# Kernel tuning notes

Measured on AMD Instinct MI355X. Metric: run time of the kernel, lower is better.

Reference implementation:

```python
import jax, jax.numpy as jnp
import numpy as np

EMBED_DIM = 2048
NUM_HEADS = 16
HEAD_DIM = EMBED_DIM // NUM_HEADS
WINDOW = 512  # window_size; also used as chunk size (S must be a multiple)


def setup_inputs() -> dict:
    key = jax.random.key(0)
    k1, k2, k3 = jax.random.split(key, 3)
    B, S = 2, 4096
    x = jax.random.normal(k1, (B, S, EMBED_DIM), dtype=jnp.float32)
    w_qkv = jax.random.normal(k2, (3 * EMBED_DIM, EMBED_DIM), dtype=jnp.float32) * 0.02
    w_out = jax.random.normal(k3, (EMBED_DIM, EMBED_DIM), dtype=jnp.float32) * 0.02
    return {"x": x, "w_qkv": w_qkv, "w_out": w_out}


def _sliding_window_attn(q, k, v, window):
    # q,k,v: [B,H,S,d]; causal sliding window: kv valid iff 0 <= q_idx - kv_idx <= window.
    # Chunked O(S*window): each query chunk of size C=window attends to its own
    # chunk and the previous one (exactly covers the band of width window+1).
    B, H, S, d = q.shape
    C = window
    nc = S // C
    qc = q.reshape(B, H, nc, C, d)

    def two_chunks(t):
        tc = t.reshape(B, H, nc, C, d)
        prev = jnp.pad(tc[:, :, :-1], ((0, 0), (0, 0), (1, 0), (0, 0), (0, 0)))
        return jnp.concatenate([prev, tc], axis=3)  # [B,H,nc,2C,d]

    kc = two_chunks(k)
    vc = two_chunks(v)

    scale = 1.0 / np.sqrt(d).astype(np.float32)
    scores = jnp.einsum('bhnid,bhnjd->bhnij', qc, kc) * scale  # [B,H,nc,C,2C]

    i = jnp.arange(C)[:, None]            # local query index
    j = jnp.arange(2 * C)[None, :]        # local kv index within the 2-chunk span
    band = (j >= i) & (j <= i + C)        # causal & within window (C == window)
    kv_global = (jnp.arange(nc)[:, None, None] - 1) * C + j[None]  # [nc,1,2C]
    mask = band[None] & (kv_global >= 0)  # [nc,C,2C]; drops padded chunk 0 keys

    scores = jnp.where(mask[None, None], scores, jnp.finfo(scores.dtype).min)
    probs = jax.nn.softmax(scores, axis=-1)
    out = jnp.einsum('bhnij,bhnjd->bhnid', probs, vc)  # [B,H,nc,C,d]
    return out.reshape(B, H, S, d)


def reference(x, w_qkv, w_out):
    B, S, E = x.shape
    qkv = jnp.einsum('bse,fe->bsf', x, w_qkv)                       # [B,S,3E]
    qkv = qkv.reshape(B, S, 3, NUM_HEADS, HEAD_DIM)
    qkv = jnp.transpose(qkv, (2, 0, 3, 1, 4))                        # [3,B,H,S,d]
    q, k, v = qkv[0], qkv[1], qkv[2]
    attn = _sliding_window_attn(q, k, v, WINDOW)                     # [B,H,S,d]
    attn = jnp.transpose(attn, (0, 2, 1, 3)).reshape(B, S, E)
    return jnp.einsum('bse,fe->bsf', attn, w_out)
```

## Files before the change

### kernel.cpp

```cpp
#include <hip/hip_runtime.h>
#include <hip/hip_bf16.h>
#include <math.h>


#define SEQ   4096
#define BATCH 2
#define EMBED 2048
#define HEADS 16
#define HDIM  128
#define NELEM (BATCH * SEQ * EMBED)
#define SCL2E (0.088388347648318447f * 1.4426950408889634f)

typedef __attribute__((ext_vector_type(8))) short short8;
typedef __attribute__((ext_vector_type(4))) float f32x4;

__device__ __forceinline__ unsigned short f2bf(float f) {
    unsigned int u = __float_as_uint(f);
    u = (u + 0x7fff + ((u >> 16) & 1)) >> 16;
    return (unsigned short)u;
}

__device__ __forceinline__ unsigned int cvt_pk_bf16(float a, float b) {
    unsigned int r;
    asm volatile("v_cvt_pk_bf16_f32 %0, %1, %2" : "=v"(r) : "v"(a), "v"(b));
    return r;
}

__global__ void cast_bf16_kernel(const float* __restrict__ src,
                                 unsigned short* __restrict__ dst, int n8)
{
    const int i = blockIdx.x * blockDim.x + threadIdx.x;
    if (i >= n8) return;
    const float4 v0 = ((const float4*)src)[2 * i];
    const float4 v1 = ((const float4*)src)[2 * i + 1];
    union { unsigned short us[8]; uint4 u4; } o;
    o.us[0] = f2bf(v0.x); o.us[1] = f2bf(v0.y); o.us[2] = f2bf(v0.z); o.us[3] = f2bf(v0.w);
    o.us[4] = f2bf(v1.x); o.us[5] = f2bf(v1.y); o.us[6] = f2bf(v1.z); o.us[7] = f2bf(v1.w);
    ((uint4*)dst)[i] = o.u4;
}

template <int MODE>
__global__ __launch_bounds__(512, 2)
void gemm256_kernel(const unsigned short* __restrict__ A,
                    const unsigned short* __restrict__ B,
                    float* __restrict__ C,
                    unsigned short* __restrict__ P0,
                    unsigned short* __restrict__ P1,
                    int M, int N, int K)
{
    __shared__ __align__(16) char lds[131072];

    const int tid  = threadIdx.x;
    const int lane = tid & 63;
    const int w    = tid >> 6;
    const int wm   = w >> 2;
    const int wn   = w & 3;
    const int l16  = lane & 15;
    const int kg   = lane >> 4;

    const int nwg  = gridDim.x * gridDim.y;
    const int bidl = blockIdx.y * gridDim.x + blockIdx.x;
    const int cpx  = nwg >> 3;
    const int swzb = (bidl & 7) * cpx + (bidl >> 3);
    const int MB   = gridDim.y;
    const int n0   = (swzb / MB) * 256;
    const int m0   = (swzb % MB) * 256;

    const int srow = w * 8 + (lane >> 3);
    const int sch8 = ((lane & 7) ^ (lane >> 3)) * 8;

    auto stage = [&](const unsigned short* X, int rowbase, int t2, int ldsbase) {
#pragma unroll
        for (int u = 0; u < 2; ++u) {
            const unsigned short* g = X + (size_t)(rowbase + u * 64 + srow) * K
                                      + t2 * 64 + sch8;
            unsigned int lb = __builtin_amdgcn_readfirstlane(
                (unsigned int)(uintptr_t)(lds + ldsbase + u * 8192 + w * 1024));
            asm volatile("s_mov_b32 m0, %0\n\t"
                         "global_load_lds_dwordx4 %1, off"
                         :: "s"(lb), "v"(g) : "memory");
        }
    };
    auto rdA = [&](int p, int mf, int ks) -> short8 {
        return *(const short8*)(lds + p * 32768 + (wm * 128 + mf * 16 + l16) * 128
                                + (((ks * 4 + kg) ^ (l16 & 7)) << 4));
    };
    auto rdB = [&](int p, int nf, int ks) -> short8 {
        return *(const short8*)(lds + 65536 + p * 32768
                                + (wn * 64 + nf * 16 + l16) * 128
                                + (((ks * 4 + kg) ^ (l16 & 7)) << 4));
    };

    f32x4 acc[8][4];
#pragma unroll
    for (int i = 0; i < 8; ++i)
#pragma unroll
        for (int j = 0; j < 4; ++j) acc[i][j] = (f32x4)0.f;

    const int NT = K >> 6;

    stage(A, m0 + 0,   0, 0);
    stage(A, m0 + 128, 0, 16384);
    stage(B, n0 + 0,   0, 65536);
    stage(B, n0 + 128, 0, 65536 + 16384);
    if (NT > 1) {
        stage(B, n0 + 0,   1, 65536 + 32768);
        stage(B, n0 + 128, 1, 65536 + 32768 + 16384);
        asm volatile("s_waitcnt vmcnt(4)" ::: "memory");
    } else {
        asm volatile("s_waitcnt vmcnt(0)" ::: "memory");
    }
    asm volatile("s_barrier" ::: "memory");

    short8 afrA[2][2], afrB[2][2], bfr[4][2];
#pragma unroll
    for (int i = 0; i < 2; ++i)
#pragma unroll
        for (int ks = 0; ks < 2; ++ks) afrA[i][ks] = rdA(0, i, ks);
#pragma unroll
    for (int nf = 0; nf < 4; ++nf)
#pragma unroll
        for (int ks = 0; ks < 2; ++ks) bfr[nf][ks] = rdB(0, nf, ks);

#define MFMA_QUAD(Q, FR)                                                        \
    __builtin_amdgcn_s_setprio(1);                                              \
    _Pragma("unroll")                                                           \
    for (int i = 0; i < 2; ++i)                                                 \
        _Pragma("unroll")                                                       \
        for (int nf = 0; nf < 4; ++nf)                                          \
            _Pragma("unroll")                                                   \
            for (int ks = 0; ks < 2; ++ks)                                      \
                acc[2 * (Q) + i][nf] = __builtin_amdgcn_mfma_f32_16x16x32_bf16( \
                    FR[i][ks], bfr[nf][ks], acc[2 * (Q) + i][nf], 0, 0, 0);     \
    __builtin_amdgcn_s_setprio(0);

    for (int t = 0; t < NT; ++t) {
        const int p = t & 1;
        if (t + 1 < NT) stage(A, m0 + 0, t + 1, (p ^ 1) * 32768);
        asm volatile("s_barrier" ::: "memory");
#pragma unroll
        for (int i = 0; i < 2; ++i)
#pragma unroll
            for (int ks = 0; ks < 2; ++ks) afrB[i][ks] = rdA(p, 2 + i, ks);
        MFMA_QUAD(0, afrA)
        if (t + 1 < NT) stage(A, m0 + 128, t + 1, (p ^ 1) * 32768 + 16384);
        asm volatile("s_barrier" ::: "memory");
#pragma unroll
        for (int i = 0; i < 2; ++i)
#pragma unroll
            for (int ks = 0; ks < 2; ++ks) afrA[i][ks] = rdA(p, 4 + i, ks);
        MFMA_QUAD(1, afrB)
        if (t + 2 < NT) stage(B, n0 + 0, t + 2, 65536 + p * 32768);
        asm volatile("s_barrier" ::: "memory");
#pragma unroll
        for (int i = 0; i < 2; ++i)
#pragma unroll
            for (int ks = 0; ks < 2; ++ks) afrB[i][ks] = rdA(p, 6 + i, ks);
        MFMA_QUAD(2, afrA)
        if (t + 2 < NT) {
            stage(B, n0 + 128, t + 2, 65536 + p * 32768 + 16384);
            asm volatile("s_waitcnt vmcnt(4)" ::: "memory");
        } else {
            asm volatile("s_waitcnt vmcnt(0)" ::: "memory");
        }
        asm volatile("s_barrier" ::: "memory");
        if (t + 1 < NT) {
#pragma unroll
            for (int i = 0; i < 2; ++i)
#pragma unroll
                for (int ks = 0; ks < 2; ++ks) afrA[i][ks] = rdA(p ^ 1, i, ks);
        }
        MFMA_QUAD(3, afrB)
        if (t + 1 < NT) {
#pragma unroll
            for (int nf = 0; nf < 4; ++nf)
#pragma unroll
                for (int ks = 0; ks < 2; ++ks) bfr[nf][ks] = rdB(p ^ 1, nf, ks);
        }
    }
#undef MFMA_QUAD

    if (MODE == 1) {
        const int cb = n0 + wn * 64;
        unsigned short* dst = (cb >> 11) ? P1 : P0;
        const int h  = (cb >> 7) & 15;
        const int db = cb & 127;
#pragma unroll
        for (int fi = 0; fi < 8; ++fi)
#pragma unroll
            for (int r = 0; r < 4; ++r) {
                const int mrow = m0 + wm * 128 + fi * 16 + kg * 4 + r;
                const int b = mrow >> 12, s = mrow & 4095;
                unsigned short* drow = dst + ((size_t)((b << 4) + h) * SEQ + s) * HDIM
                                       + db + l16;
#pragma unroll
                for (int nf = 0; nf < 4; ++nf) drow[nf * 16] = f2bf(acc[fi][nf][r]);
            }
    } else if (MODE == 2) {
#pragma unroll
        for (int fi = 0; fi < 8; ++fi)
#pragma unroll
            for (int r = 0; r < 4; ++r) {
                const int mrow = m0 + wm * 128 + fi * 16 + kg * 4 + r;
                const int h = mrow >> 7, d = mrow & 127;
#pragma unroll
                for (int nf = 0; nf < 4; ++nf) {
                    const int col = n0 + wn * 64 + nf * 16 + l16;
                    const int b = col >> 12, s = col & 4095;
                    const int sl = s & 63;
                    const int c = (sl & 0x23) | ((sl & 0x0C) << 1) | ((sl & 0x10) >> 2);
                    P0[((size_t)((b << 4) + h) * HDIM + d) * SEQ + (s & ~63) + c] =
                        f2bf(acc[fi][nf][r]);
                }
            }
    } else {
#pragma unroll
        for (int fi = 0; fi < 8; ++fi)
#pragma unroll
            for (int r = 0; r < 4; ++r) {
                float* crow = C + (size_t)(m0 + wm * 128 + fi * 16 + kg * 4 + r) * N
                              + n0 + wn * 64 + l16;
#pragma unroll
                for (int nf = 0; nf < 4; ++nf) crow[nf * 16] = acc[fi][nf][r];
            }
    }
}

__global__ __launch_bounds__(512)
void swa_mfma_kernel(const unsigned short* __restrict__ Qg,
                     const unsigned short* __restrict__ Kg,
                     const unsigned short* __restrict__ Vtg,
                     unsigned short* __restrict__ O )
{
    __shared__ __align__(16) char lds[65536];

    const int bid = blockIdx.x;
    const int qt  = bid & 31;
    const int h   = (bid >> 5) & 15;
    const int b   = bid >> 9;
    const int q0  = qt * 128;
    const int tid  = threadIdx.x;
    const int w    = tid >> 6;
    const int lane = tid & 63;
    const int l16  = lane & 15;
    const int kg   = lane >> 4;
    const size_t base = (size_t)((b << 4) + h) * SEQ * HDIM;
    const int gq = q0 + w * 16 + l16;

    short8 qf[4];
#pragma unroll
    for (int kw = 0; kw < 4; ++kw)
        qf[kw] = *(const short8*)(Qg + base + (size_t)gq * HDIM + kw * 32 + kg * 8);

    f32x4 acc_o[8];
#pragma unroll
    for (int db = 0; db < 8; ++db) acc_o[db] = (f32x4)0.f;
    float m = -1e30f, l = 0.f;

    auto stageKV = [&](int kt, int buf) {
        const int gk0 = q0 - 512 + kt * 64;
#pragma unroll
        for (int u = 0; u < 2; ++u) {
            {
                const int id  = u * 512 + w * 64 + lane;
                const int row = id >> 4, ch = id & 15;
                const char* g = (const char*)(Kg + base + (size_t)(gk0 + row) * HDIM
                                              + ((ch ^ (row & 7)) << 3));
                unsigned int lb = __builtin_amdgcn_readfirstlane(
                    (unsigned int)(uintptr_t)(lds + buf * 32768 + u * 8192 + w * 1024));
                asm volatile("s_mov_b32 m0, %0\n\t"
                             "global_load_lds_dwordx4 %1, off"
                             :: "s"(lb), "v"(g) : "memory");
            }
            {
                const int id  = u * 512 + w * 64 + lane;
                const int d   = id >> 3, ch = id & 7;
                const char* g = (const char*)(Vtg + base + (size_t)d * SEQ + gk0
                                              + ((ch ^ (d & 7)) << 3));
                unsigned int lb = __builtin_amdgcn_readfirstlane(
                    (unsigned int)(uintptr_t)(lds + buf * 32768 + 16384
                                              + u * 8192 + w * 1024));
                asm volatile("s_mov_b32 m0, %0\n\t"
                             "global_load_lds_dwordx4 %1, off"
                             :: "s"(lb), "v"(g) : "memory");
            }
        }
    };

    const int kt_start = (qt < 4) ? (8 - 2 * qt) : 0;
    stageKV(kt_start, 0);
    int cur = 0;

    for (int kt = kt_start; kt < 10; ++kt) {
        asm volatile("s_waitcnt vmcnt(0)" ::: "memory");
        __syncthreads();
        if (kt + 1 < 10) stageKV(kt + 1, cur ^ 1);

        const int gk0 = q0 - 512 + kt * 64;
        const char* ldsb = lds + cur * 32768;
        const int qlo = q0 + w * 16;
        const bool active = (gk0 <= qlo + 15) && (gk0 + 63 >= qlo - 512);
        if (active) {
            f32x4 s4[4];
#pragma unroll
            for (int kb = 0; kb < 4; ++kb) s4[kb] = (f32x4)0.f;
#pragma unroll
            for (int kw = 0; kw < 4; ++kw)
#pragma unroll
                for (int kb = 0; kb < 4; ++kb) {
                    short8 kf = *(const short8*)(ldsb + (kb * 16 + l16) * 256
                                                 + (((kw * 4 + kg) ^ (l16 & 7)) << 4));
                    s4[kb] = __builtin_amdgcn_mfma_f32_16x16x32_bf16(
                        kf, qf[kw], s4[kb], 0, 0, 0);
                }

            const int dq = gq - gk0;
            float p[4][4];
            float tm = -1e30f;
#pragma unroll
            for (int kb = 0; kb < 4; ++kb)
#pragma unroll
                for (int r = 0; r < 4; ++r) {
                    const int koff = kb * 16 + kg * 4 + r;
                    const bool valid = (koff <= dq) && (koff >= dq - 512);
                    const float sv = valid ? s4[kb][r] * SCL2E : -1e30f;
                    p[kb][r] = sv;
                    tm = fmaxf(tm, sv);
                }
            tm = fmaxf(tm, __shfl_xor(tm, 16));
            tm = fmaxf(tm, __shfl_xor(tm, 32));
            const float mn   = fmaxf(m, tm);
            const float corr = __builtin_amdgcn_exp2f(m - mn);
            m = mn;
            l *= corr;
            float cr[4];
#pragma unroll
            for (int r = 0; r < 4; ++r) cr[r] = __shfl(corr, kg * 4 + r);
#pragma unroll
            for (int db = 0; db < 8; ++db)
#pragma unroll
                for (int r = 0; r < 4; ++r) acc_o[db][r] *= cr[r];

            float ts = 0.f;
#pragma unroll
            for (int kb = 0; kb < 4; ++kb)
#pragma unroll
                for (int r = 0; r < 4; ++r) {
                    const float pv = (p[kb][r] > -1e29f)
                                         ? __builtin_amdgcn_exp2f(p[kb][r] - m) : 0.f;
                    p[kb][r] = pv;
                    ts += pv;
                }
            ts += __shfl_xor(ts, 16);
            ts += __shfl_xor(ts, 32);
            l += ts;

            unsigned int dw[4][2];
#pragma unroll
            for (int kb = 0; kb < 4; ++kb) {
                dw[kb][0] = cvt_pk_bf16(p[kb][0], p[kb][1]);
                dw[kb][1] = cvt_pk_bf16(p[kb][2], p[kb][3]);
            }
#pragma unroll
            for (int w2 = 0; w2 < 2; ++w2) {
                union { unsigned int u[4]; short8 v; } pu;
                pu.u[0] = dw[2 * w2][0];     pu.u[1] = dw[2 * w2][1];
                pu.u[2] = dw[2 * w2 + 1][0]; pu.u[3] = dw[2 * w2 + 1][1];
#pragma unroll
                for (int db = 0; db < 8; ++db) {
                    short8 vf = *(const short8*)(ldsb + 16384 + (db * 16 + l16) * 128
                                                 + (((w2 * 4 + kg) ^ (l16 & 7)) << 4));
                    acc_o[db] = __builtin_amdgcn_mfma_f32_16x16x32_bf16(
                        pu.v, vf, acc_o[db], 0, 0, 0);
                }
            }
        }
        cur ^= 1;
    }

    const float inv = 1.0f / l;
    float li[4];
#pragma unroll
    for (int r = 0; r < 4; ++r) li[r] = __shfl(inv, kg * 4 + r);
#pragma unroll
    for (int db = 0; db < 8; ++db)
#pragma unroll
        for (int r = 0; r < 4; ++r) {
            const int gqr = q0 + w * 16 + kg * 4 + r;
            O[((size_t)b * SEQ + gqr) * EMBED + h * HDIM + db * 16 + l16] =
                f2bf(acc_o[db][r] * li[r]);
        }
}

extern "C" void kernel_launch(void* const* d_in, const int* in_sizes, int n_in,
                              void* d_out, int out_size, void* d_ws, size_t ws_size,
                              hipStream_t stream)
{
    const float* x     = (const float*)d_in[0];
    const float* w_qkv = (const float*)d_in[1];
    const float* w_out = (const float*)d_in[2];
    float* out = (float*)d_out;

    char* ws = (char*)d_ws;
    unsigned short* xb    = (unsigned short*)(ws);
    unsigned short* wqkvb = (unsigned short*)(ws + 33554432);
    unsigned short* woutb = (unsigned short*)(ws + 58720256);
    unsigned short* qb    = (unsigned short*)(ws + 67108864);
    unsigned short* kb    = (unsigned short*)(ws + 100663296);
    unsigned short* vtb   = (unsigned short*)(ws + 134217728);
    unsigned short* attnb = (unsigned short*)(ws + 167772160);

    const int M = BATCH * SEQ;
    dim3 blk(256);

    hipLaunchKernelGGL(cast_bf16_kernel, dim3(NELEM / 8 / 256), blk, 0, stream,
                       x, xb, NELEM / 8);
    hipLaunchKernelGGL(cast_bf16_kernel, dim3(3 * EMBED * EMBED / 8 / 256), blk, 0, stream,
                       w_qkv, wqkvb, 3 * EMBED * EMBED / 8);
    hipLaunchKernelGGL(cast_bf16_kernel, dim3(EMBED * EMBED / 8 / 256), blk, 0, stream,
                       w_out, woutb, EMBED * EMBED / 8);

    hipLaunchKernelGGL((gemm256_kernel<1>), dim3(16, 32), dim3(512), 0, stream,
                       xb, wqkvb, (float*)nullptr, qb, kb, M, 2 * EMBED, EMBED);

    hipLaunchKernelGGL((gemm256_kernel<2>), dim3(32, 8), dim3(512), 0, stream,
                       wqkvb + (size_t)2 * EMBED * EMBED, xb, (float*)nullptr,
                       vtb, (unsigned short*)nullptr, EMBED, M, EMBED);

    hipLaunchKernelGGL(swa_mfma_kernel, dim3(BATCH * HEADS * (SEQ / 128)), dim3(512),
                       0, stream, qb, kb, vtb, attnb);

    hipLaunchKernelGGL((gemm256_kernel<0>), dim3(8, 32), dim3(512), 0, stream,
                       attnb, woutb, out, (unsigned short*)nullptr,
                       (unsigned short*)nullptr, M, EMBED, EMBED);
}
```

Before: 356.1 us.

## Restructure GEMM main loop to single-buffer fragments with barriers around each MFMA quad

The GEMM main loop drops the register double-buffering of A fragments (afrA/afrB) and the prefetch of next-tile fragments. It now loads fragments for each quad just before its MFMAs, with explicit lgkmcnt waits and a barrier before and after every MFMA block. The block-to-tile mapping is also changed to row-major over gridDim.x instead of column-major over gridDim.y. This cuts register pressure and tightens scheduling, but it exposes LDS read latency and adds roughly twice as many barriers per iteration.

Result: slower. 365.7 us (+2.7%).

```diff
diff --git a/kernel.cpp b/kernel.cpp
--- a/kernel.cpp
+++ b/kernel.cpp
@@ -62,9 +62,8 @@
     const int bidl = blockIdx.y * gridDim.x + blockIdx.x;
     const int cpx  = nwg >> 3;
     const int swzb = (bidl & 7) * cpx + (bidl >> 3);
-    const int MB   = gridDim.y;
-    const int n0   = (swzb / MB) * 256;
-    const int m0   = (swzb % MB) * 256;
+    const int m0   = (swzb / gridDim.x) * 256;
+    const int n0   = (swzb % gridDim.x) * 256;
 
     const int srow = w * 8 + (lane >> 3);
     const int sch8 = ((lane & 7) ^ (lane >> 3)) * 8;
@@ -110,19 +109,11 @@
     } else {
         asm volatile("s_waitcnt vmcnt(0)" ::: "memory");
     }
-    asm volatile("s_barrier" ::: "memory");
-
-    short8 afrA[2][2], afrB[2][2], bfr[4][2];
-#pragma unroll
-    for (int i = 0; i < 2; ++i)
-#pragma unroll
-        for (int ks = 0; ks < 2; ++ks) afrA[i][ks] = rdA(0, i, ks);
-#pragma unroll
-    for (int nf = 0; nf < 4; ++nf)
-#pragma unroll
-        for (int ks = 0; ks < 2; ++ks) bfr[nf][ks] = rdB(0, nf, ks);
-
-#define MFMA_QUAD(Q, FR)                                                        \
+    __builtin_amdgcn_s_barrier();
+
+    short8 afr[2][2], bfr[4][2];
+
+#define MFMA_QUAD(Q)                                                            \
     __builtin_amdgcn_s_setprio(1);                                              \
     _Pragma("unroll")                                                           \
     for (int i = 0; i < 2; ++i)                                                 \
@@ -131,52 +122,54 @@
             _Pragma("unroll")                                                   \
             for (int ks = 0; ks < 2; ++ks)                                      \
                 acc[2 * (Q) + i][nf] = __builtin_amdgcn_mfma_f32_16x16x32_bf16( \
-                    FR[i][ks], bfr[nf][ks], acc[2 * (Q) + i][nf], 0, 0, 0);     \
+                    afr[i][ks], bfr[nf][ks], acc[2 * (Q) + i][nf], 0, 0, 0);    \
     __builtin_amdgcn_s_setprio(0);
 
     for (int t = 0; t < NT; ++t) {
         const int p = t & 1;
+#pragma unroll
+        for (int i = 0; i < 2; ++i)
+#pragma unroll
+            for (int ks = 0; ks < 2; ++ks) afr[i][ks] = rdA(p, i, ks);
+#pragma unroll
+        for (int nf = 0; nf < 4; ++nf)
+#pragma unroll
+            for (int ks = 0; ks < 2; ++ks) bfr[nf][ks] = rdB(p, nf, ks);
         if (t + 1 < NT) stage(A, m0 + 0, t + 1, (p ^ 1) * 32768);
-        asm volatile("s_barrier" ::: "memory");
+        asm volatile("s_waitcnt lgkmcnt(8)" ::: "memory");
+        __builtin_amdgcn_s_barrier();
+        asm volatile("s_waitcnt lgkmcnt(0)" ::: "memory");
+        MFMA_QUAD(0)
+        __builtin_amdgcn_s_barrier();
 #pragma unroll
         for (int i = 0; i < 2; ++i)
 #pragma unroll
-            for (int ks = 0; ks < 2; ++ks) afrB[i][ks] = rdA(p, 2 + i, ks);
-        MFMA_QUAD(0, afrA)
+            for (int ks = 0; ks < 2; ++ks) afr[i][ks] = rdA(p, 2 + i, ks);
         if (t + 1 < NT) stage(A, m0 + 128, t + 1, (p ^ 1) * 32768 + 16384);
-        asm volatile("s_barrier" ::: "memory");
+        __builtin_amdgcn_s_barrier();
+        asm volatile("s_waitcnt lgkmcnt(0)" ::: "memory");
+        MFMA_QUAD(1)
+        __builtin_amdgcn_s_barrier();
 #pragma unroll
         for (int i = 0; i < 2; ++i)
 #pragma unroll
-            for (int ks = 0; ks < 2; ++ks) afrA[i][ks] = rdA(p, 4 + i, ks);
-        MFMA_QUAD(1, afrB)
+            for (int ks = 0; ks < 2; ++ks) afr[i][ks] = rdA(p, 4 + i, ks);
         if (t + 2 < NT) stage(B, n0 + 0, t + 2, 65536 + p * 32768);
-        asm volatile("s_barrier" ::: "memory");
+        __builtin_amdgcn_s_barrier();
+        asm volatile("s_waitcnt lgkmcnt(0)" ::: "memory");
+        MFMA_QUAD(2)
+        __builtin_amdgcn_s_barrier();
 #pragma unroll
         for (int i = 0; i < 2; ++i)
 #pragma unroll
-            for (int ks = 0; ks < 2; ++ks) afrB[i][ks] = rdA(p, 6 + i, ks);
-        MFMA_QUAD(2, afrA)
-        if (t + 2 < NT) {
-            stage(B, n0 + 128, t + 2, 65536 + p * 32768 + 16384);
-            asm volatile("s_waitcnt vmcnt(4)" ::: "memory");
-        } else {
-            asm volatile("s_waitcnt vmcnt(0)" ::: "memory");
-        }
-        asm volatile("s_barrier" ::: "memory");
-        if (t + 1 < NT) {
-#pragma unroll
-            for (int i = 0; i < 2; ++i)
-#pragma unroll
-                for (int ks = 0; ks < 2; ++ks) afrA[i][ks] = rdA(p ^ 1, i, ks);
-        }
-        MFMA_QUAD(3, afrB)
-        if (t + 1 < NT) {
-#pragma unroll
-            for (int nf = 0; nf < 4; ++nf)
-#pragma unroll
-                for (int ks = 0; ks < 2; ++ks) bfr[nf][ks] = rdB(p ^ 1, nf, ks);
-        }
+            for (int ks = 0; ks < 2; ++ks) afr[i][ks] = rdA(p, 6 + i, ks);
+        if (t + 2 < NT) stage(B, n0 + 128, t + 2, 65536 + p * 32768 + 16384);
+        if (t >= NT - 2) asm volatile("s_waitcnt vmcnt(0)" ::: "memory");
+        else             asm volatile("s_waitcnt vmcnt(4)" ::: "memory");
+        __builtin_amdgcn_s_barrier();
+        asm volatile("s_waitcnt lgkmcnt(0)" ::: "memory");
+        MFMA_QUAD(3)
+        __builtin_amdgcn_s_barrier();
     }
 #undef MFMA_QUAD
 
```
